# Kernel tuning notes

Hardware: AMD Instinct MI355X
Metric: run time of the kernel (lower is better)

Reference implementation:

```python
import jax, jax.numpy as jnp
import numpy as np

T, B, I, H = 512, 32, 512, 512

def setup_inputs() -> dict:
    key = jax.random.key(0)
    k1, k2, k3 = jax.random.split(key, 3)
    x = jax.random.normal(k1, (T, B, I), dtype=jnp.float32)
    h0 = jnp.zeros((B, H), dtype=jnp.float32)
    W_ih = jax.random.normal(k2, (3 * H, I), dtype=jnp.float32) * (1.0 / np.sqrt(H))
    # diagonal recurrent weights, one vector per gate (r, z, n), uniform(-1, 1)
    w_hh = jax.random.uniform(k3, (3, H), dtype=jnp.float32, minval=-1.0, maxval=1.0)
    return {"x": x, "h0": h0, "W_ih": W_ih, "w_hh": w_hh}

def reference(x, h0, W_ih, w_hh):
    # Precompute input-side gate pre-activations for all timesteps: (T, B, 3H)
    gx = jnp.einsum('tbi,gi->tbg', x, W_ih)
    xr, xz, xn = jnp.split(gx, 3, axis=-1)  # each (T, B, H)
    w_r, w_z, w_n = w_hh[0], w_hh[1], w_hh[2]  # each (H,)

    def step(h, g):
        gr, gz, gn = g
        r = jax.nn.sigmoid(gr + w_r * h)
        z = jax.nn.sigmoid(gz + w_z * h)
        n = jnp.tanh(gn + r * (w_n * h))
        h_new = (1.0 - z) * n + z * h
        return h_new, h_new

    h_last, out = jax.lax.scan(step, h0, (xr, xz, xn))
    # out: (T, B, H) all hidden states; h_last: (1, B, H) final state (GRU convention)
    return out, h_last[None, :, :]
```

## Files before the change

kernel.cpp:

```cpp
#include <hip/hip_runtime.h>
#include <hip/hip_bf16.h>
#include <stdint.h>

#define T_DIM 512
#define B_DIM 32
#define K_DIM 512
#define H_DIM 512
#define N_DIM 1536
#define M_DIM 16384

typedef __bf16 bf16_t;
typedef bf16_t bf16x8 __attribute__((ext_vector_type(8)));
typedef float floatx4 __attribute__((ext_vector_type(4)));

__device__ __forceinline__ unsigned int f2bf_bits(float f) {
  uint32_t u = __builtin_bit_cast(uint32_t, f);
  u += 0x7FFFu + ((u >> 16) & 1u);
  return u >> 16;
}

__global__ void convert_bf16_kernel(const float* __restrict__ in,
                                    unsigned short* __restrict__ out, int n) {
  int i = (blockIdx.x * blockDim.x + threadIdx.x) * 8;
  if (i >= n) return;
  const float4* p = (const float4*)(in + i);
  float4 f0 = p[0];
  float4 f1 = p[1];
  uint4 v;
  v.x = f2bf_bits(f0.x) | (f2bf_bits(f0.y) << 16);
  v.y = f2bf_bits(f0.z) | (f2bf_bits(f0.w) << 16);
  v.z = f2bf_bits(f1.x) | (f2bf_bits(f1.y) << 16);
  v.w = f2bf_bits(f1.z) | (f2bf_bits(f1.w) << 16);
  *(uint4*)(out + i) = v;
}

__global__ __launch_bounds__(256) void gemm_bf16_kernel(
    const unsigned short* __restrict__ A, const unsigned short* __restrict__ Bm,
    float* __restrict__ C) {
  __shared__ bf16_t smem[16384];
  const int tid = threadIdx.x;
  const int lane = tid & 63;
  const int w = tid >> 6;
  const int tileM = blockIdx.x * 128;
  const int tileN = blockIdx.y * 128;
  const int waveM = w & 1;
  const int waveN = w >> 1;
  const int lm = lane & 15;
  const int lg = lane >> 4;

  floatx4 acc[4][4] = {};

  for (int k0 = 0; k0 < K_DIM; k0 += 64) {
#pragma unroll
    for (int j = 0; j < 4; ++j) {
      int s = j * 256 + tid;
      int row = s >> 3;
      int cpos = s & 7;
      int kc = cpos ^ (row & 7);
      bf16_t* la = smem + (j * 256 + w * 64) * 8;
      const unsigned short* ga = A + (size_t)(tileM + row) * K_DIM + k0 + kc * 8;
      __builtin_amdgcn_global_load_lds(
          (const __attribute__((address_space(1))) unsigned int*)ga,
          (__attribute__((address_space(3))) unsigned int*)la, 16, 0, 0);
      bf16_t* lb = smem + 8192 + (j * 256 + w * 64) * 8;
      const unsigned short* gb = Bm + (size_t)(tileN + row) * K_DIM + k0 + kc * 8;
      __builtin_amdgcn_global_load_lds(
          (const __attribute__((address_space(1))) unsigned int*)gb,
          (__attribute__((address_space(3))) unsigned int*)lb, 16, 0, 0);
    }
    __syncthreads();

#pragma unroll
    for (int ks = 0; ks < 2; ++ks) {
      bf16x8 af[4], bfg[4];
#pragma unroll
      for (int i = 0; i < 4; ++i) {
        int row = waveM * 64 + i * 16 + lm;
        int c = ks * 4 + lg;
        af[i] = *(const bf16x8*)(smem + row * 64 + (c ^ (row & 7)) * 8);
      }
#pragma unroll
      for (int j = 0; j < 4; ++j) {
        int row = waveN * 64 + j * 16 + lm;
        int c = ks * 4 + lg;
        bfg[j] = *(const bf16x8*)(smem + 8192 + row * 64 + (c ^ (row & 7)) * 8);
      }
#pragma unroll
      for (int i = 0; i < 4; ++i)
#pragma unroll
        for (int j = 0; j < 4; ++j)
          acc[i][j] = __builtin_amdgcn_mfma_f32_16x16x32_bf16(af[i], bfg[j],
                                                              acc[i][j], 0, 0, 0);
    }
    __syncthreads();
  }

  const int row0 = tileM + waveM * 64 + (lane >> 4) * 4;
  const int col0 = tileN + waveN * 64 + lm;
#pragma unroll
  for (int i = 0; i < 4; ++i)
#pragma unroll
    for (int j = 0; j < 4; ++j)
#pragma unroll
      for (int r = 0; r < 4; ++r)
        C[(size_t)(row0 + i * 16 + r) * N_DIM + col0 + j * 16] = acc[i][j][r];
}

__device__ __forceinline__ float fast_sigmoid(float x) {
  float e = __builtin_amdgcn_exp2f(-1.442695041f * x);
  return __builtin_amdgcn_rcpf(1.0f + e);
}
__device__ __forceinline__ float fast_tanh(float x) {
  float e = __builtin_amdgcn_exp2f(2.885390082f * x);
  return 1.0f - 2.0f * __builtin_amdgcn_rcpf(e + 1.0f);
}

__global__ __launch_bounds__(64) void indgru_scan_kernel(
    const float* __restrict__ gx, const float* __restrict__ h0,
    const float* __restrict__ w_hh, float* __restrict__ out,
    float* __restrict__ hlast) {
  const int idx = blockIdx.x * 64 + threadIdx.x;
  const int b = idx >> 9;
  const int h = idx & (H_DIM - 1);
  const float wr = w_hh[h];
  const float wz = w_hh[H_DIM + h];
  const float wn = w_hh[2 * H_DIM + h];
  float hv = h0[idx];

  const float* base = gx + (size_t)b * N_DIM + h;
  float* outp = out + (size_t)b * H_DIM + h;

  constexpr int D = 16;
  float pr[D], pz[D], pn[D];
#pragma unroll
  for (int t = 0; t < D; ++t) {
    const float* p = base + (size_t)t * (B_DIM * N_DIM);
    pr[t] = p[0];
    pz[t] = p[H_DIM];
    pn[t] = p[2 * H_DIM];
  }

  for (int t0 = 0; t0 < T_DIM - D; t0 += D) {
#pragma unroll
    for (int s = 0; s < D; ++s) {
      const int t = t0 + s;
      float gr = pr[s], gz = pz[s], gn = pn[s];
      const float* p = base + (size_t)(t + D) * (B_DIM * N_DIM);
      pr[s] = p[0];
      pz[s] = p[H_DIM];
      pn[s] = p[2 * H_DIM];
      float r = fast_sigmoid(gr + wr * hv);
      float z = fast_sigmoid(gz + wz * hv);
      float n = fast_tanh(gn + r * (wn * hv));
      hv = (1.0f - z) * n + z * hv;
      outp[(size_t)t * (B_DIM * H_DIM)] = hv;
    }
  }
#pragma unroll
  for (int s = 0; s < D; ++s) {
    const int t = T_DIM - D + s;
    float r = fast_sigmoid(pr[s] + wr * hv);
    float z = fast_sigmoid(pz[s] + wz * hv);
    float n = fast_tanh(pn[s] + r * (wn * hv));
    hv = (1.0f - z) * n + z * hv;
    outp[(size_t)t * (B_DIM * H_DIM)] = hv;
  }
  hlast[idx] = hv;
}

extern "C" void kernel_launch(void* const* d_in, const int* in_sizes, int n_in,
                              void* d_out, int out_size, void* d_ws, size_t ws_size,
                              hipStream_t stream) {
  const float* x    = (const float*)d_in[0];
  const float* h0   = (const float*)d_in[1];
  const float* W_ih = (const float*)d_in[2];
  const float* w_hh = (const float*)d_in[3];

  float* out = (float*)d_out;
  float* hlast = out + (size_t)T_DIM * B_DIM * H_DIM;

  char* ws = (char*)d_ws;
  unsigned short* xb = (unsigned short*)ws;
  unsigned short* Wb = (unsigned short*)(ws + 16777216);
  float* gx = (float*)(ws + 16777216 + 1572864);

  convert_bf16_kernel<<<4096, 256, 0, stream>>>(x, xb, M_DIM * K_DIM);
  convert_bf16_kernel<<<384, 256, 0, stream>>>(W_ih, Wb, N_DIM * K_DIM);

  dim3 grid(M_DIM / 128, N_DIM / 128);
  gemm_bf16_kernel<<<grid, 256, 0, stream>>>(xb, Wb, gx);

  indgru_scan_kernel<<<256, 64, 0, stream>>>(gx, h0, w_hh, out, hlast);
}
```

Before: 176.5 us.

## Fold exp2 scaling constants into GEMM epilogue and recurrent weights; merge convert kernels

```diff
diff --git a/kernel.cpp b/kernel.cpp
--- a/kernel.cpp
+++ b/kernel.cpp
@@ -13,16 +13,28 @@
 typedef bf16_t bf16x8 __attribute__((ext_vector_type(8)));
 typedef float floatx4 __attribute__((ext_vector_type(4)));
 
+#define LOG2E 1.442695041f
+#define TWO_LOG2E 2.885390082f
+
 __device__ __forceinline__ unsigned int f2bf_bits(float f) {
   uint32_t u = __builtin_bit_cast(uint32_t, f);
   u += 0x7FFFu + ((u >> 16) & 1u);
   return u >> 16;
 }
 
-__global__ void convert_bf16_kernel(const float* __restrict__ in,
-                                    unsigned short* __restrict__ out, int n) {
-  int i = (blockIdx.x * blockDim.x + threadIdx.x) * 8;
-  if (i >= n) return;
+__global__ void convert_both_kernel(const float* __restrict__ x,
+                                    unsigned short* __restrict__ xb,
+                                    const float* __restrict__ W,
+                                    unsigned short* __restrict__ Wb) {
+  int bid = blockIdx.x;
+  const float* in;
+  unsigned short* out;
+  int i;
+  if (bid < 4096) {
+    in = x; out = xb; i = (bid * 256 + threadIdx.x) * 8;
+  } else {
+    in = W; out = Wb; i = ((bid - 4096) * 256 + threadIdx.x) * 8;
+  }
   const float4* p = (const float4*)(in + i);
   float4 f0 = p[0];
   float4 f1 = p[1];
@@ -100,19 +112,13 @@
 #pragma unroll
   for (int i = 0; i < 4; ++i)
 #pragma unroll
-    for (int j = 0; j < 4; ++j)
+    for (int j = 0; j < 4; ++j) {
+      const int col = col0 + j * 16;
+      const float scl = (col >= 2 * H_DIM) ? TWO_LOG2E : -LOG2E;
 #pragma unroll
       for (int r = 0; r < 4; ++r)
-        C[(size_t)(row0 + i * 16 + r) * N_DIM + col0 + j * 16] = acc[i][j][r];
-}
-
-__device__ __forceinline__ float fast_sigmoid(float x) {
-  float e = __builtin_amdgcn_exp2f(-1.442695041f * x);
-  return __builtin_amdgcn_rcpf(1.0f + e);
-}
-__device__ __forceinline__ float fast_tanh(float x) {
-  float e = __builtin_amdgcn_exp2f(2.885390082f * x);
-  return 1.0f - 2.0f * __builtin_amdgcn_rcpf(e + 1.0f);
+        C[(size_t)(row0 + i * 16 + r) * N_DIM + col] = scl * acc[i][j][r];
+    }
 }
 
 __global__ __launch_bounds__(64) void indgru_scan_kernel(
@@ -122,12 +128,12 @@
   const int idx = blockIdx.x * 64 + threadIdx.x;
   const int b = idx >> 9;
   const int h = idx & (H_DIM - 1);
-  const float wr = w_hh[h];
-  const float wz = w_hh[H_DIM + h];
-  const float wn = w_hh[2 * H_DIM + h];
+  const float wr = -LOG2E * w_hh[h];
+  const float wz = -LOG2E * w_hh[H_DIM + h];
+  const float wn = TWO_LOG2E * w_hh[2 * H_DIM + h];
   float hv = h0[idx];
 
-  const float* base = gx + (size_t)b * N_DIM + h;
+  const float* base = gx + (size_t)b * N_DIM + H_DIM + h;
   float* outp = out + (size_t)b * H_DIM + h;
 
   constexpr int D = 16;
@@ -135,9 +141,9 @@
 #pragma unroll
   for (int t = 0; t < D; ++t) {
     const float* p = base + (size_t)t * (B_DIM * N_DIM);
-    pr[t] = p[0];
-    pz[t] = p[H_DIM];
-    pn[t] = p[2 * H_DIM];
+    pr[t] = p[-H_DIM];
+    pz[t] = p[0];
+    pn[t] = p[H_DIM];
   }
 
   for (int t0 = 0; t0 < T_DIM - D; t0 += D) {
@@ -146,23 +152,41 @@
       const int t = t0 + s;
       float gr = pr[s], gz = pz[s], gn = pn[s];
       const float* p = base + (size_t)(t + D) * (B_DIM * N_DIM);
-      pr[s] = p[0];
-      pz[s] = p[H_DIM];
-      pn[s] = p[2 * H_DIM];
-      float r = fast_sigmoid(gr + wr * hv);
-      float z = fast_sigmoid(gz + wz * hv);
-      float n = fast_tanh(gn + r * (wn * hv));
-      hv = (1.0f - z) * n + z * hv;
+      pr[s] = p[-H_DIM];
+      pz[s] = p[0];
+      pn[s] = p[H_DIM];
+      float ar = fmaf(wr, hv, gr);
+      float az = fmaf(wz, hv, gz);
+      float t1 = wn * hv;
+      float er = __builtin_amdgcn_exp2f(ar);
+      float ez = __builtin_amdgcn_exp2f(az);
+      float r = __builtin_amdgcn_rcpf(1.0f + er);
+      float z = __builtin_amdgcn_rcpf(1.0f + ez);
+      float en = __builtin_amdgcn_exp2f(fmaf(r, t1, gn));
+      float u = __builtin_amdgcn_rcpf(1.0f + en);
+      float n = fmaf(-2.0f, u, 1.0f);
+      float zh = z * hv;
+      float omz = 1.0f - z;
+      hv = fmaf(n, omz, zh);
       outp[(size_t)t * (B_DIM * H_DIM)] = hv;
     }
   }
 #pragma unroll
   for (int s = 0; s < D; ++s) {
     const int t = T_DIM - D + s;
-    float r = fast_sigmoid(pr[s] + wr * hv);
-    float z = fast_sigmoid(pz[s] + wz * hv);
-    float n = fast_tanh(pn[s] + r * (wn * hv));
-    hv = (1.0f - z) * n + z * hv;
+    float ar = fmaf(wr, hv, pr[s]);
+    float az = fmaf(wz, hv, pz[s]);
+    float t1 = wn * hv;
+    float er = __builtin_amdgcn_exp2f(ar);
+    float ez = __builtin_amdgcn_exp2f(az);
+    float r = __builtin_amdgcn_rcpf(1.0f + er);
+    float z = __builtin_amdgcn_rcpf(1.0f + ez);
+    float en = __builtin_amdgcn_exp2f(fmaf(r, t1, pn[s]));
+    float u = __builtin_amdgcn_rcpf(1.0f + en);
+    float n = fmaf(-2.0f, u, 1.0f);
+    float zh = z * hv;
+    float omz = 1.0f - z;
+    hv = fmaf(n, omz, zh);
     outp[(size_t)t * (B_DIM * H_DIM)] = hv;
   }
   hlast[idx] = hv;
@@ -184,8 +208,7 @@
   unsigned short* Wb = (unsigned short*)(ws + 16777216);
   float* gx = (float*)(ws + 16777216 + 1572864);
 
-  convert_bf16_kernel<<<4096, 256, 0, stream>>>(x, xb, M_DIM * K_DIM);
-  convert_bf16_kernel<<<384, 256, 0, stream>>>(W_ih, Wb, N_DIM * K_DIM);
+  convert_both_kernel<<<4480, 256, 0, stream>>>(x, xb, W_ih, Wb);
 
   dim3 grid(M_DIM / 128, N_DIM / 128);
   gemm_bf16_kernel<<<grid, 256, 0, stream>>>(xb, Wb, gx);
```

Measured after the change: 172.3 us. 2.4% less time.
